# Optimization experiments

Measured on AMD Instinct MI355X. Metric: run time of the kernel, lower is better.

Reference implementation:

```python
import jax, jax.numpy as jnp
import numpy as np

B, Z, H, T = 256, 512, 2048, 16
EPS = 1e-5

def _normalize(v):
    return v / (jnp.linalg.norm(v) + 1e-12)

def setup_inputs() -> dict:
    key = jax.random.key(0)
    ks = jax.random.split(key, 10)
    s = lambda fan: 1.0 / np.sqrt(fan)
    return {
        "z": jax.random.normal(ks[0], (B, Z), dtype=jnp.float32),
        "fc_w": jax.random.normal(ks[1], (Z, Z), dtype=jnp.float32) * s(Z),
        "fc_b": jnp.zeros((Z,), dtype=jnp.float32),
        "fc_u": _normalize(jax.random.normal(ks[2], (Z,), dtype=jnp.float32)),
        "w_ih": jax.random.normal(ks[3], (3 * H, Z), dtype=jnp.float32) * s(Z),
        "w_hh": jax.random.normal(ks[4], (3 * H, H), dtype=jnp.float32) * s(H),
        "b_ih": jnp.zeros((3 * H,), dtype=jnp.float32).at[H:2 * H].set(1.0),  # forget-gate bias init
        "b_hh": jnp.zeros((3 * H,), dtype=jnp.float32),
        "lin_w": jax.random.normal(ks[5], (Z, H), dtype=jnp.float32) * s(H),
        "lin_b": jnp.zeros((Z,), dtype=jnp.float32),
    }

def _spectral_norm(w, u):
    # one torch-style power iteration (u, v treated as constants)
    v = jax.lax.stop_gradient(_normalize(w.T @ u))
    u1 = jax.lax.stop_gradient(_normalize(w @ v))
    sigma = u1 @ (w @ v)
    return w / sigma

def reference(z, fc_w, fc_b, fc_u, w_ih, w_hh, b_ih, b_hh, lin_w, lin_b):
    # spectral-norm linear: h0 = z @ (W/sigma)^T + b
    w_sn = _spectral_norm(fc_w, fc_u)
    x0 = z @ w_sn.T + fc_b                      # [B, Z]
    h0 = jnp.zeros((B, H), dtype=z.dtype)       # initHidden

    def step(carry, _):
        x, h = carry
        gi = x @ w_ih.T + b_ih                  # [B, 3H]
        gh = h @ w_hh.T + b_hh                  # [B, 3H]
        i_r, i_z, i_n = jnp.split(gi, 3, axis=1)
        h_r, h_z, h_n = jnp.split(gh, 3, axis=1)
        r = jax.nn.sigmoid(i_r + h_r)
        u = jax.nn.sigmoid(i_z + h_z)
        n = jnp.tanh(i_n + r * h_n)
        h_new = (1.0 - u) * n + u * h
        x_new = h_new @ lin_w.T + lin_b         # [B, Z] fed back as next input
        return (x_new, h_new), x_new

    _, outs = jax.lax.scan(step, (x0, h0), None, length=T)  # [T, B, Z]

    # per-timestep BatchNorm1d(affine=False), training-mode batch stats
    mean = jnp.mean(outs, axis=1, keepdims=True)
    var = jnp.mean((outs - mean) ** 2, axis=1, keepdims=True)
    y = (outs - mean) / jnp.sqrt(var + EPS)     # [T, B, Z]

    y = jnp.transpose(y, (1, 0, 2))             # [B, T, Z]
    return y.reshape(-1, Z)                     # [B*T, Z]
```

## Files before the change

kernel.cpp:

```cpp
#include <hip/hip_runtime.h>
#include <hip/hip_bf16.h>
#include <cstdint>
#include <cstddef>

#define B_  256
#define Z_  512
#define H_  2048
#define T_  16
#define H3_ 6144

using short8  = __attribute__((ext_vector_type(8))) short;
using bf16x8  = __attribute__((ext_vector_type(8))) __bf16;
using f32x4   = __attribute__((ext_vector_type(4))) float;
using f32x16  = __attribute__((ext_vector_type(16))) float;

__device__ __forceinline__ f32x4 mfma_bf16(short8 a, short8 b, f32x4 c) {
  return __builtin_amdgcn_mfma_f32_16x16x32_bf16(
      __builtin_bit_cast(bf16x8, a), __builtin_bit_cast(bf16x8, b), c, 0, 0, 0);
}
__device__ __forceinline__ f32x16 mfma_bf16_32(short8 a, short8 b, f32x16 c) {
  return __builtin_amdgcn_mfma_f32_32x32x16_bf16(
      __builtin_bit_cast(bf16x8, a), __builtin_bit_cast(bf16x8, b), c, 0, 0, 0);
}

__device__ __forceinline__ unsigned short f2bf(float f) {
  unsigned int u = __builtin_bit_cast(unsigned int, f);
  u = (u + 0x7FFFu + ((u >> 16) & 1u)) >> 16;
  return (unsigned short)u;
}

__device__ __forceinline__ float sigmoidf_(float x) { return 1.0f / (1.0f + __expf(-x)); }

__device__ __forceinline__ int swz(int row, int chunk) {
  return row * 64 + ((chunk ^ (row & 7)) << 3);
}

__global__ __launch_bounds__(256, 1) void gru_step5(
    const unsigned short* __restrict__ A, int K,
    const unsigned short* __restrict__ Wr,
    const unsigned short* __restrict__ Wz,
    const unsigned short* __restrict__ Wn,
    const unsigned short* __restrict__ Whn,
    const float* __restrict__ cr, const float* __restrict__ cz,
    const float* __restrict__ cn, const float* __restrict__ chn,
    float hn_scale,
    const float* __restrict__ h_old,
    float* __restrict__ h_new,
    unsigned short* __restrict__ h_hist)
{
  __shared__ __align__(16) unsigned short sbuf[2][12288];
  __shared__ float LDSf[4][64][33];
  const int bid = blockIdx.x, tid = threadIdx.x;
  const int xcd = bid & 7, rst = bid >> 3;
  const int m_idx = rst & 3, gg = rst >> 2;
  const int grp = gg * 8 + xcd;
  const int m0 = m_idx * 64;
  const int gh0 = grp * 32;
  const int wave = tid >> 6, lane = tid & 63;
  const int kk = wave & 1, gp = wave >> 1;
  const int lh = lane >> 5, l31 = lane & 31;

  const int arow = tid >> 2, ac0 = (tid & 3) * 2;
  const int wrow = tid >> 1, wc0 = (tid & 1) * 4;
  const unsigned short* wsrc =
      (wave == 0) ? Wr : (wave == 1) ? Wz : (wave == 2) ? Wn : Whn;
  const size_t aoff = (size_t)(m0 + arow) * K + ac0 * 8;
  const size_t woff = (size_t)(gh0 + (wrow & 31)) * K + wc0 * 8;
  const int sa_d0 = swz(arow, ac0);
  const int sa_d1 = swz(arow, ac0 + 1);
  const int sw_d0 = 4096 + swz(wrow, wc0 + 0);
  const int sw_d1 = 4096 + swz(wrow, wc0 + 1);
  const int sw_d2 = 4096 + swz(wrow, wc0 + 2);
  const int sw_d3 = 4096 + swz(wrow, wc0 + 3);

  uint4 Aa0, Aa1, Aw0, Aw1, Aw2, Aw3;
  uint4 Ba0, Ba1, Bw0, Bw1, Bw2, Bw3;

#define LDSET(a0, a1, w0, w1, w2, w3, k0)                  \
  {                                                        \
    const int kk_ = (k0);                                  \
    a0 = *(const uint4*)(A    + aoff + kk_);               \
    a1 = *(const uint4*)(A    + aoff + kk_ + 8);           \
    w0 = *(const uint4*)(wsrc + woff + kk_);               \
    w1 = *(const uint4*)(wsrc + woff + kk_ + 8);           \
    w2 = *(const uint4*)(wsrc + woff + kk_ + 16);          \
    w3 = *(const uint4*)(wsrc + woff + kk_ + 24);          \
  }
#define STAGE(s, a0, a1, w0, w1, w2, w3)                   \
  {                                                        \
    unsigned short* b_ = sbuf[s];                          \
    *(uint4*)(b_ + sa_d0) = a0;                            \
    *(uint4*)(b_ + sa_d1) = a1;                            \
    *(uint4*)(b_ + sw_d0) = w0;                            \
    *(uint4*)(b_ + sw_d1) = w1;                            \
    *(uint4*)(b_ + sw_d2) = w2;                            \
    *(uint4*)(b_ + sw_d3) = w3;                            \
  }

  f32x16 acc00 = {}, acc01 = {}, acc10 = {}, acc11 = {};
  const int g0r = (gp * 2) * 32, g1r = (gp * 2 + 1) * 32;

#define COMP(s)                                                            \
  {                                                                        \
    const unsigned short* b_ = sbuf[s];                                    \
    _Pragma("unroll")                                                      \
    for (int ksi = 0; ksi < 2; ++ksi) {                                    \
      const int ch = kk * 4 + ksi * 2 + lh;                                \
      short8 af0 = *(const short8*)(b_ + swz(l31, ch));                    \
      short8 af1 = *(const short8*)(b_ + swz(32 + l31, ch));               \
      short8 wf0 = *(const short8*)(b_ + 4096 + swz(g0r + l31, ch));       \
      short8 wf1 = *(const short8*)(b_ + 4096 + swz(g1r + l31, ch));       \
      acc00 = mfma_bf16_32(af0, wf0, acc00);                               \
      acc01 = mfma_bf16_32(af0, wf1, acc01);                               \
      acc10 = mfma_bf16_32(af1, wf0, acc10);                               \
      acc11 = mfma_bf16_32(af1, wf1, acc11);                               \
    }                                                                      \
  }

  const int nIter = K >> 6;
  LDSET(Aa0, Aa1, Aw0, Aw1, Aw2, Aw3, 0);
  LDSET(Ba0, Ba1, Bw0, Bw1, Bw2, Bw3, 64);
  for (int it = 0; it < nIter; it += 2) {
    STAGE(0, Aa0, Aa1, Aw0, Aw1, Aw2, Aw3);
    __syncthreads();
    { const int kn = (it + 2 < nIter) ? ((it + 2) << 6) : 0;
      LDSET(Aa0, Aa1, Aw0, Aw1, Aw2, Aw3, kn); }
    COMP(0);
    STAGE(1, Ba0, Ba1, Bw0, Bw1, Bw2, Bw3);
    __syncthreads();
    { const int kn = (it + 3 < nIter) ? ((it + 3) << 6) : 64;
      LDSET(Ba0, Ba1, Bw0, Bw1, Bw2, Bw3, kn); }
    COMP(1);
  }
#undef LDSET
#undef STAGE
#undef COMP

  __syncthreads();
  float* red = (float*)sbuf;
#define RSLOT(t, r) ((((gp << 2) | (t)) * 16 + (r)) * 64 + lane)
  if (kk == 1) {
#pragma unroll
    for (int r = 0; r < 16; ++r) red[RSLOT(0, r)] = acc00[r];
#pragma unroll
    for (int r = 0; r < 16; ++r) red[RSLOT(1, r)] = acc01[r];
#pragma unroll
    for (int r = 0; r < 16; ++r) red[RSLOT(2, r)] = acc10[r];
#pragma unroll
    for (int r = 0; r < 16; ++r) red[RSLOT(3, r)] = acc11[r];
  }
  __syncthreads();
  if (kk == 0) {
#pragma unroll
    for (int r = 0; r < 16; ++r) acc00[r] += red[RSLOT(0, r)];
#pragma unroll
    for (int r = 0; r < 16; ++r) acc01[r] += red[RSLOT(1, r)];
#pragma unroll
    for (int r = 0; r < 16; ++r) acc10[r] += red[RSLOT(2, r)];
#pragma unroll
    for (int r = 0; r < 16; ++r) acc11[r] += red[RSLOT(3, r)];
#pragma unroll
    for (int r = 0; r < 16; ++r) {
      const int trow = (r & 3) + 8 * (r >> 2) + 4 * lh;
      LDSf[gp * 2    ][trow     ][l31] = acc00[r];
      LDSf[gp * 2 + 1][trow     ][l31] = acc01[r];
      LDSf[gp * 2    ][32 + trow][l31] = acc10[r];
      LDSf[gp * 2 + 1][32 + trow][l31] = acc11[r];
    }
  }
#undef RSLOT
  __syncthreads();
  {
    const int row = tid >> 2, c0 = (tid & 3) * 8;
    const int grow = m0 + row;
#pragma unroll
    for (int j = 0; j < 8; ++j) {
      const int col = c0 + j;
      const int gcol = gh0 + col;
      const float R   = sigmoidf_(LDSf[0][row][col] + cr[gcol]);
      const float U   = sigmoidf_(LDSf[1][row][col] + cz[gcol]);
      const float HNv = hn_scale * LDSf[3][row][col] + chn[gcol];
      const float Nv  = tanhf(LDSf[2][row][col] + cn[gcol] + R * HNv);
      const float ho  = h_old ? h_old[(size_t)grow * H_ + gcol] : 0.0f;
      const float hv  = (1.0f - U) * Nv + U * ho;
      h_new[(size_t)grow * H_ + gcol]  = hv;
      h_hist[(size_t)grow * H_ + gcol] = f2bf(hv);
    }
  }
}

__global__ __launch_bounds__(256) void gemm_bt(
    const unsigned short* __restrict__ A,
    const unsigned short* __restrict__ Bw,
    int K,
    const float* __restrict__ addsrc, int add_ld,
    const float* __restrict__ bias,
    const float* __restrict__ scale_ptr,
    unsigned short* __restrict__ out_bf,
    float* __restrict__ out_f, int ldo)
{
  __shared__ unsigned short sA[32 * 64];
  __shared__ unsigned short sB[64 * 64];
  const int tid  = threadIdx.x;
  const int m0   = blockIdx.x * 32, n0 = blockIdx.y * 64;
  const int wave = tid >> 6, lane = tid & 63;
  const int wr = wave & 1, wc = wave >> 1;
  const int q = lane >> 4, c16 = lane & 15;
  const int lr = tid >> 3, lc8 = tid & 7;
  f32x4 acc0 = {}, acc1 = {};
  const size_t rowA  = (size_t)(m0 + lr) * K;
  const size_t rowB0 = (size_t)(n0 + lr) * K;
  const size_t rowB1 = (size_t)(n0 + 32 + lr) * K;
  for (int k0 = 0; k0 < K; k0 += 64) {
    const int gc = k0 + lc8 * 8;
    uint4 ra  = *(const uint4*)(A  + rowA  + gc);
    uint4 rb0 = *(const uint4*)(Bw + rowB0 + gc);
    uint4 rb1 = *(const uint4*)(Bw + rowB1 + gc);
    __syncthreads();
    *(uint4*)(sA + swz(lr, lc8))      = ra;
    *(uint4*)(sB + swz(lr, lc8))      = rb0;
    *(uint4*)(sB + swz(32 + lr, lc8)) = rb1;
    __syncthreads();
#pragma unroll
    for (int kk = 0; kk < 2; ++kk) {
      const int arow = wr * 16 + c16;
      short8 af = *(const short8*)(sA + swz(arow, kk * 4 + q));
      const int brow = wc * 32 + c16;
      short8 b0 = *(const short8*)(sB + swz(brow, kk * 4 + q));
      acc0 = mfma_bf16(af, b0, acc0);
      short8 b1 = *(const short8*)(sB + swz(brow + 16, kk * 4 + q));
      acc1 = mfma_bf16(af, b1, acc1);
    }
  }
  const float scale = scale_ptr ? *scale_ptr : 1.0f;
#pragma unroll
  for (int cf = 0; cf < 2; ++cf) {
    f32x4 a = cf ? acc1 : acc0;
#pragma unroll
    for (int v = 0; v < 4; ++v) {
      const int row = m0 + wr * 16 + q * 4 + v;
      const int col = n0 + wc * 32 + cf * 16 + c16;
      float val = a[v] * scale;
      if (addsrc) val += addsrc[(size_t)row * add_ld + col];
      if (bias)   val += bias[col];
      if (out_f)  out_f[(size_t)row * ldo + col] = val;
      if (out_bf) out_bf[(size_t)row * ldo + col] = f2bf(val);
    }
  }
}

__device__ __forceinline__ void dev_gemm64core(
    unsigned short* sA, unsigned short* sB,
    const unsigned short* __restrict__ A,
    const unsigned short* __restrict__ Bw,
    int K,
    const float* __restrict__ addsrc, int add_ld,
    const float* __restrict__ bias,
    unsigned short* __restrict__ out_bf,
    float* __restrict__ out_f, int ldo, int mi, int ni)
{
  const int tid  = threadIdx.x;
  const int m0   = mi * 64, n0 = ni * 64;
  const int wave = tid >> 6, lane = tid & 63;
  const int wr = wave & 1, wc = wave >> 1;
  const int q = lane >> 4, c16 = lane & 15;
  const int lr = tid >> 3, lc8 = tid & 7;
  f32x4 acc[2][2] = {};
  const size_t aoff = (size_t)(m0 + lr) * K;
  const size_t boff = (size_t)(n0 + lr) * K;
  const size_t s32  = (size_t)32 * K;

  uint4 ra0, ra1, rb0, rb1;
  auto LOAD = [&](int k0) {
    const int gc = k0 + lc8 * 8;
    ra0 = *(const uint4*)(A  + aoff + gc);
    ra1 = *(const uint4*)(A  + aoff + s32 + gc);
    rb0 = *(const uint4*)(Bw + boff + gc);
    rb1 = *(const uint4*)(Bw + boff + s32 + gc);
  };

  const int nIter = K >> 6;
  LOAD(0);
  for (int it = 0; it < nIter; ++it) {
    __syncthreads();
    *(uint4*)(sA + swz(lr, lc8))      = ra0;
    *(uint4*)(sA + swz(lr + 32, lc8)) = ra1;
    *(uint4*)(sB + swz(lr, lc8))      = rb0;
    *(uint4*)(sB + swz(lr + 32, lc8)) = rb1;
    __syncthreads();
    if (it + 1 < nIter) LOAD((it + 1) << 6);
#pragma unroll
    for (int kk = 0; kk < 2; ++kk) {
      short8 af0 = *(const short8*)(sA + swz(wr * 32 + c16,      kk * 4 + q));
      short8 af1 = *(const short8*)(sA + swz(wr * 32 + 16 + c16, kk * 4 + q));
      short8 bf0 = *(const short8*)(sB + swz(wc * 32 + c16,      kk * 4 + q));
      short8 bf1 = *(const short8*)(sB + swz(wc * 32 + 16 + c16, kk * 4 + q));
      acc[0][0] = mfma_bf16(af0, bf0, acc[0][0]);
      acc[0][1] = mfma_bf16(af0, bf1, acc[0][1]);
      acc[1][0] = mfma_bf16(af1, bf0, acc[1][0]);
      acc[1][1] = mfma_bf16(af1, bf1, acc[1][1]);
    }
  }
#pragma unroll
  for (int i = 0; i < 2; ++i) {
#pragma unroll
    for (int j = 0; j < 2; ++j) {
#pragma unroll
      for (int v = 0; v < 4; ++v) {
        const int row = m0 + wr * 32 + i * 16 + q * 4 + v;
        const int col = n0 + wc * 32 + j * 16 + c16;
        float val = acc[i][j][v];
        if (addsrc) val += addsrc[(size_t)row * add_ld + col];
        if (bias)   val += bias[col];
        if (out_f)  out_f[(size_t)row * ldo + col] = val;
        if (out_bf) out_bf[(size_t)row * ldo + col] = f2bf(val);
      }
    }
  }
}

__global__ __launch_bounds__(256) void gemm_bt64(
    const unsigned short* __restrict__ A,
    const unsigned short* __restrict__ Bw,
    int K,
    const float* __restrict__ addsrc, int add_ld,
    const float* __restrict__ bias,
    unsigned short* __restrict__ out_bf,
    float* __restrict__ out_f, int ldo)
{
  __shared__ unsigned short sA[64 * 64];
  __shared__ unsigned short sB[64 * 64];
  dev_gemm64core(sA, sB, A, Bw, K, addsrc, add_ld, bias, out_bf, out_f, ldo,
                 blockIdx.x, blockIdx.y);
}

__global__ __launch_bounds__(256) void gemm_wsum(
    const unsigned short* __restrict__ w_ih_q,
    const unsigned short* __restrict__ lin_wT_q,
    const float* __restrict__ w_hh,
    unsigned short* __restrict__ Wsum_r,
    unsigned short* __restrict__ Wsum_z,
    unsigned short* __restrict__ Wn_c)
{
  __shared__ unsigned short sA[64 * 64];
  __shared__ unsigned short sB[64 * 64];
  const int g = blockIdx.y >> 5, ni = blockIdx.y & 31;
  const float* adds = (g < 2) ? (w_hh + (size_t)g * H_ * H_) : nullptr;
  unsigned short* outw = (g == 0) ? Wsum_r : (g == 1) ? Wsum_z : Wn_c;
  dev_gemm64core(sA, sB, w_ih_q + (size_t)g * H_ * Z_, lin_wT_q, Z_,
                 adds, H_, nullptr, outw, nullptr, H_, blockIdx.x, ni);
}

__global__ __launch_bounds__(256) void quant_all(
    const float* __restrict__ z, const float* __restrict__ fc_w,
    const float* __restrict__ w_ih, const float* __restrict__ w_hh,
    const float* __restrict__ lin_w,
    unsigned short* __restrict__ z_q, unsigned short* __restrict__ fc_w_q,
    unsigned short* __restrict__ w_ih_q, unsigned short* __restrict__ w_hhn_q,
    unsigned short* __restrict__ lin_w_q)
{
  const int i = blockIdx.x * 256 + threadIdx.x;
  if (i >= 2195456) return;
  const float4* src; ushort4* dst; int idx;
  if (i < 32768)        { src = (const float4*)z;     dst = (ushort4*)z_q;     idx = i; }
  else if (i < 98304)   { src = (const float4*)fc_w;  dst = (ushort4*)fc_w_q;  idx = i - 32768; }
  else if (i < 884736)  { src = (const float4*)w_ih;  dst = (ushort4*)w_ih_q;  idx = i - 98304; }
  else if (i < 1933312) { src = (const float4*)(w_hh + (size_t)2 * H_ * H_);
                          dst = (ushort4*)w_hhn_q;    idx = i - 884736; }
  else                  { src = (const float4*)lin_w; dst = (ushort4*)lin_w_q; idx = i - 1933312; }
  float4 v = src[idx];
  ushort4 o; o.x = f2bf(v.x); o.y = f2bf(v.y); o.z = f2bf(v.z); o.w = f2bf(v.w);
  dst[idx] = o;
}

__global__ __launch_bounds__(256) void transq(const float* __restrict__ s,
                                              unsigned short* __restrict__ d) {
  __shared__ float tile[32][33];
  const int tx = threadIdx.x & 31, ty = threadIdx.x >> 5;
  const int k0 = blockIdx.x * 32, z0 = blockIdx.y * 32;
#pragma unroll
  for (int j = 0; j < 4; ++j)
    tile[ty + j * 8][tx] = s[(size_t)(z0 + ty + j * 8) * H_ + k0 + tx];
  __syncthreads();
#pragma unroll
  for (int j = 0; j < 4; ++j)
    d[(size_t)(k0 + ty + j * 8) * Z_ + z0 + tx] = f2bf(tile[tx][ty + j * 8]);
}

__global__ void sigma1(const float* __restrict__ W, const float* __restrict__ u,
                       float* __restrict__ t1) {
  __shared__ float part[4][64];
  const int lane = threadIdx.x & 63, wv = threadIdx.x >> 6;
  const int col = blockIdx.x * 64 + lane;
  float s = 0.f;
  for (int r = wv * 128; r < wv * 128 + 128; ++r)
    s += W[(size_t)r * Z_ + col] * u[r];
  part[wv][lane] = s;
  __syncthreads();
  if (wv == 0)
    t1[col] = part[0][lane] + part[1][lane] + part[2][lane] + part[3][lane];
}

__global__ void sigma2(const float* __restrict__ W, const float* __restrict__ t1,
                       float* __restrict__ t2) {
  __shared__ float red[256];
  const int tid = threadIdx.x;
  float p = 0.f;
  for (int c = tid; c < Z_; c += 256) { float v = t1[c]; p += v * v; }
  red[tid] = p;
  __syncthreads();
  for (int s = 128; s > 0; s >>= 1) {
    if (tid < s) red[tid] += red[tid + s];
    __syncthreads();
  }
  const float invn = 1.0f / (sqrtf(red[0]) + 1e-12f);
  const int lane = tid & 63, wv = tid >> 6;
  const int row = blockIdx.x * 4 + wv;
  float s = 0.f;
  for (int c = lane; c < Z_; c += 64) s += W[(size_t)row * Z_ + c] * t1[c];
#pragma unroll
  for (int off = 32; off > 0; off >>= 1) s += __shfl_down(s, off);
  if (lane == 0) t2[row] = s * invn;
}

__global__ void sigma3(const float* __restrict__ t2, float* __restrict__ inv_sig) {
  __shared__ float red[256];
  int t = threadIdx.x;
  float v0 = t2[t], v1 = t2[t + 256];
  red[t] = v0 * v0 + v1 * v1;
  __syncthreads();
  for (int s = 128; s > 0; s >>= 1) {
    if (t < s) red[t] += red[t + s];
    __syncthreads();
  }
  if (t == 0) {
    float s2  = red[0];
    float sig = s2 / (sqrtf(s2) + 1e-12f);
    inv_sig[0] = 1.0f / sig;
  }
}

__global__ __launch_bounds__(256) void dots2_k(
    const float* __restrict__ w, const float* __restrict__ lb,
    const float* __restrict__ b_ih, const float* __restrict__ b_hh,
    float* __restrict__ c0r, float* __restrict__ c0z, float* __restrict__ c0n,
    float* __restrict__ c1r, float* __restrict__ c1z, float* __restrict__ c1n,
    float* __restrict__ chn)
{
  const int wave = threadIdx.x >> 6, lane = threadIdx.x & 63;
#pragma unroll
  for (int i = 0; i < 4; ++i) {
    int row = blockIdx.x * 16 + wave * 4 + i;
    float s = 0.f;
    for (int c = lane; c < Z_; c += 64) s += w[(size_t)row * Z_ + c] * lb[c];
#pragma unroll
    for (int off = 32; off > 0; off >>= 1) s += __shfl_down(s, off);
    if (lane == 0) {
      const int g = row >> 11, j = row & 2047;
      const float bi = b_ih[row], bh = b_hh[row];
      if (g == 0)      { c0r[j] = bi + bh; c1r[j] = bi + bh + s; }
      else if (g == 1) { c0z[j] = bi + bh; c1z[j] = bi + bh + s; }
      else             { c0n[j] = bi;      c1n[j] = bi + s;      chn[j] = bh; }
    }
  }
}

__global__ __launch_bounds__(256) void bn_k(const float* __restrict__ outs,
                                            float* __restrict__ y) {
  __shared__ float s_sum[4][64], s_sq[4][64], s_mean[64], s_inv[64];
  const int t = blockIdx.x, zb = blockIdx.y;
  const int zl = threadIdx.x & 63, bp = threadIdx.x >> 6;
  const int z = zb * 64 + zl;
  float sum = 0.f, sq = 0.f;
  for (int b = bp * 64; b < bp * 64 + 64; ++b) {
    float v = outs[(size_t)(t * 256 + b) * Z_ + z];
    sum += v; sq += v * v;
  }
  s_sum[bp][zl] = sum; s_sq[bp][zl] = sq;
  __syncthreads();
  if (bp == 0) {
    float S = s_sum[0][zl] + s_sum[1][zl] + s_sum[2][zl] + s_sum[3][zl];
    float Q = s_sq[0][zl] + s_sq[1][zl] + s_sq[2][zl] + s_sq[3][zl];
    float mean = S * (1.0f / 256.0f);
    float var  = Q * (1.0f / 256.0f) - mean * mean;
    s_mean[zl] = mean;
    s_inv[zl]  = rsqrtf(var + 1e-5f);
  }
  __syncthreads();
  const float mean = s_mean[zl], inv = s_inv[zl];
  for (int b = bp * 64; b < bp * 64 + 64; ++b) {
    float v = outs[(size_t)(t * 256 + b) * Z_ + z];
    y[(size_t)(b * T_ + t) * Z_ + z] = (v - mean) * inv;
  }
}

extern "C" void kernel_launch(void* const* d_in, const int* in_sizes, int n_in,
                              void* d_out, int out_size, void* d_ws, size_t ws_size,
                              hipStream_t stream) {
  const float* z     = (const float*)d_in[0];
  const float* fc_w  = (const float*)d_in[1];
  const float* fc_b  = (const float*)d_in[2];
  const float* fc_u  = (const float*)d_in[3];
  const float* w_ih  = (const float*)d_in[4];
  const float* w_hh  = (const float*)d_in[5];
  const float* b_ih  = (const float*)d_in[6];
  const float* b_hh  = (const float*)d_in[7];
  const float* lin_w = (const float*)d_in[8];
  const float* lin_b = (const float*)d_in[9];
  float* out = (float*)d_out;

  char* ws = (char*)d_ws;
  size_t off = 0;
  auto alloc = [&](size_t bytes) -> void* {
    off = (off + 255) & ~(size_t)255;
    void* p = ws + off;
    off += bytes;
    return p;
  };
  unsigned short* w_ih_q   = (unsigned short*)alloc((size_t)H3_ * Z_ * 2);
  unsigned short* w_hhn_q  = (unsigned short*)alloc((size_t)H_ * H_ * 2);
  unsigned short* lin_w_q  = (unsigned short*)alloc((size_t)Z_ * H_ * 2);
  unsigned short* lin_wT_q = (unsigned short*)alloc((size_t)Z_ * H_ * 2);
  unsigned short* fc_w_q   = (unsigned short*)alloc((size_t)Z_ * Z_ * 2);
  unsigned short* z_q      = (unsigned short*)alloc((size_t)B_ * Z_ * 2);
  unsigned short* x0_q     = (unsigned short*)alloc((size_t)B_ * Z_ * 2);
  unsigned short* Wsum_r   = (unsigned short*)alloc((size_t)H_ * H_ * 2);
  unsigned short* Wsum_z   = (unsigned short*)alloc((size_t)H_ * H_ * 2);
  unsigned short* Wn_c     = (unsigned short*)alloc((size_t)H_ * H_ * 2);
  unsigned short* Hhist    = (unsigned short*)alloc((size_t)T_ * B_ * H_ * 2);
  float* h_f32 = (float*)alloc((size_t)2 * B_ * H_ * 4);
  float* outs  = (float*)alloc((size_t)T_ * B_ * Z_ * 4);
  float* c0r = (float*)alloc(H_ * 4);
  float* c0z = (float*)alloc(H_ * 4);
  float* c0n = (float*)alloc(H_ * 4);
  float* c1r = (float*)alloc(H_ * 4);
  float* c1z = (float*)alloc(H_ * 4);
  float* c1n = (float*)alloc(H_ * 4);
  float* chn = (float*)alloc(H_ * 4);
  float* t1v = (float*)alloc(Z_ * 4);
  float* t2v = (float*)alloc(Z_ * 4);
  float* invsig = (float*)alloc(256);
  (void)in_sizes; (void)n_in; (void)out_size; (void)ws_size;

  quant_all<<<dim3((2195456 + 255) / 256), 256, 0, stream>>>(
      z, fc_w, w_ih, w_hh, lin_w, z_q, fc_w_q, w_ih_q, w_hhn_q, lin_w_q);
  transq<<<dim3(64, 16), 256, 0, stream>>>(lin_w, lin_wT_q);
  sigma1<<<8, 256, 0, stream>>>(fc_w, fc_u, t1v);
  sigma2<<<128, 256, 0, stream>>>(fc_w, t1v, t2v);
  sigma3<<<1, 256, 0, stream>>>(t2v, invsig);
  dots2_k<<<384, 256, 0, stream>>>(w_ih, lin_b, b_ih, b_hh,
                                   c0r, c0z, c0n, c1r, c1z, c1n, chn);

  gemm_bt<<<dim3(B_ / 32, Z_ / 64), 256, 0, stream>>>(
      z_q, fc_w_q, Z_, nullptr, 0, fc_b, invsig, x0_q, nullptr, Z_);

  gemm_wsum<<<dim3(H_ / 64, 96), 256, 0, stream>>>(
      w_ih_q, lin_wT_q, w_hh, Wsum_r, Wsum_z, Wn_c);

  for (int t = 0; t < T_; ++t) {
    if (t == 0) {
      gru_step5<<<256, 256, 0, stream>>>(
          x0_q, Z_,
          w_ih_q, w_ih_q + (size_t)H_ * Z_, w_ih_q + (size_t)2 * H_ * Z_,
          w_ih_q ,
          c0r, c0z, c0n, chn, 0.0f, nullptr, h_f32, Hhist);
    } else {
      gru_step5<<<256, 256, 0, stream>>>(
          Hhist + (size_t)(t - 1) * B_ * H_, H_,
          Wsum_r, Wsum_z, Wn_c, w_hhn_q,
          c1r, c1z, c1n, chn, 1.0f,
          h_f32 + (size_t)((t - 1) & 1) * B_ * H_,
          h_f32 + (size_t)(t & 1) * B_ * H_,
          Hhist + (size_t)t * B_ * H_);
    }
  }

  gemm_bt64<<<dim3(T_ * B_ / 64, Z_ / 64), 256, 0, stream>>>(
      Hhist, lin_w_q, H_, nullptr, 0, lin_b, nullptr, outs, Z_);

  bn_k<<<dim3(T_, Z_ / 64), 256, 0, stream>>>(outs, out);
}
```

Before: 446.3 us.

## Pre-pack GRU weights into MFMA fragment order and load directly to registers

Weights for the recurrent step are repacked once into the per-lane MFMA operand layout, so each wave loads its B fragments straight from global memory into registers, with no LDS staging. The step kernel goes to 512 threads, one wave per gate and K-half, and only the activation tile goes through shared memory. This removes LDS traffic and barriers for the weight stream. The cost is extra packing work in the preprocessing kernels, an extra packed copy of w_ih, and more register pressure.

```diff
diff --git a/kernel.cpp b/kernel.cpp
--- a/kernel.cpp
+++ b/kernel.cpp
@@ -35,7 +35,13 @@
   return row * 64 + ((chunk ^ (row & 7)) << 3);
 }
 
-__global__ __launch_bounds__(256, 1) void gru_step5(
+__device__ __forceinline__ size_t pidx(int row, int col, int K) {
+  const int grp = row >> 5, prow = row & 31;
+  const int s = col >> 4, lh = (col >> 3) & 1, j = col & 7;
+  return (((size_t)grp * (K >> 4) + s) << 9) + (((lh << 5) | prow) << 3) + j;
+}
+
+__global__ __launch_bounds__(512, 1) void gru_step6(
     const unsigned short* __restrict__ A, int K,
     const unsigned short* __restrict__ Wr,
     const unsigned short* __restrict__ Wz,
@@ -48,7 +54,8 @@
     float* __restrict__ h_new,
     unsigned short* __restrict__ h_hist)
 {
-  __shared__ __align__(16) unsigned short sbuf[2][12288];
+  __shared__ __align__(16) unsigned short sA[2][4096];
+  __shared__ float rawred[8][16][64];
   __shared__ float LDSf[4][64][33];
   const int bid = blockIdx.x, tid = threadIdx.x;
   const int xcd = bid & 7, rst = bid >> 3;
@@ -57,124 +64,76 @@
   const int m0 = m_idx * 64;
   const int gh0 = grp * 32;
   const int wave = tid >> 6, lane = tid & 63;
-  const int kk = wave & 1, gp = wave >> 1;
+  const int gate = wave & 3, kk = wave >> 2;
   const int lh = lane >> 5, l31 = lane & 31;
 
-  const int arow = tid >> 2, ac0 = (tid & 3) * 2;
-  const int wrow = tid >> 1, wc0 = (tid & 1) * 4;
-  const unsigned short* wsrc =
-      (wave == 0) ? Wr : (wave == 1) ? Wz : (wave == 2) ? Wn : Whn;
-  const size_t aoff = (size_t)(m0 + arow) * K + ac0 * 8;
-  const size_t woff = (size_t)(gh0 + (wrow & 31)) * K + wc0 * 8;
-  const int sa_d0 = swz(arow, ac0);
-  const int sa_d1 = swz(arow, ac0 + 1);
-  const int sw_d0 = 4096 + swz(wrow, wc0 + 0);
-  const int sw_d1 = 4096 + swz(wrow, wc0 + 1);
-  const int sw_d2 = 4096 + swz(wrow, wc0 + 2);
-  const int sw_d3 = 4096 + swz(wrow, wc0 + 3);
-
-  uint4 Aa0, Aa1, Aw0, Aw1, Aw2, Aw3;
-  uint4 Ba0, Ba1, Bw0, Bw1, Bw2, Bw3;
-
-#define LDSET(a0, a1, w0, w1, w2, w3, k0)                  \
-  {                                                        \
-    const int kk_ = (k0);                                  \
-    a0 = *(const uint4*)(A    + aoff + kk_);               \
-    a1 = *(const uint4*)(A    + aoff + kk_ + 8);           \
-    w0 = *(const uint4*)(wsrc + woff + kk_);               \
-    w1 = *(const uint4*)(wsrc + woff + kk_ + 8);           \
-    w2 = *(const uint4*)(wsrc + woff + kk_ + 16);          \
-    w3 = *(const uint4*)(wsrc + woff + kk_ + 24);          \
-  }
-#define STAGE(s, a0, a1, w0, w1, w2, w3)                   \
-  {                                                        \
-    unsigned short* b_ = sbuf[s];                          \
-    *(uint4*)(b_ + sa_d0) = a0;                            \
-    *(uint4*)(b_ + sa_d1) = a1;                            \
-    *(uint4*)(b_ + sw_d0) = w0;                            \
-    *(uint4*)(b_ + sw_d1) = w1;                            \
-    *(uint4*)(b_ + sw_d2) = w2;                            \
-    *(uint4*)(b_ + sw_d3) = w3;                            \
-  }
-
-  f32x16 acc00 = {}, acc01 = {}, acc10 = {}, acc11 = {};
-  const int g0r = (gp * 2) * 32, g1r = (gp * 2 + 1) * 32;
-
-#define COMP(s)                                                            \
-  {                                                                        \
-    const unsigned short* b_ = sbuf[s];                                    \
-    _Pragma("unroll")                                                      \
-    for (int ksi = 0; ksi < 2; ++ksi) {                                    \
-      const int ch = kk * 4 + ksi * 2 + lh;                                \
-      short8 af0 = *(const short8*)(b_ + swz(l31, ch));                    \
-      short8 af1 = *(const short8*)(b_ + swz(32 + l31, ch));               \
-      short8 wf0 = *(const short8*)(b_ + 4096 + swz(g0r + l31, ch));       \
-      short8 wf1 = *(const short8*)(b_ + 4096 + swz(g1r + l31, ch));       \
-      acc00 = mfma_bf16_32(af0, wf0, acc00);                               \
-      acc01 = mfma_bf16_32(af0, wf1, acc01);                               \
-      acc10 = mfma_bf16_32(af1, wf0, acc10);                               \
-      acc11 = mfma_bf16_32(af1, wf1, acc11);                               \
-    }                                                                      \
-  }
+  const unsigned short* Wg =
+      (gate == 0) ? Wr : (gate == 1) ? Wz : (gate == 2) ? Wn : Whn;
+  const int ns = K >> 4;
+  const unsigned short* wbase = Wg + (((size_t)grp * ns) << 9) + lane * 8;
+
+  const int arow = tid >> 3, achk = tid & 7;
+  const size_t aoff = (size_t)(m0 + arow) * K + achk * 8;
+  const int sa_d = swz(arow, achk);
+
+  f32x16 acc0 = {}, acc1 = {};
+  uint4 Ar, W0, W1, Wn0, Wn1;
 
   const int nIter = K >> 6;
-  LDSET(Aa0, Aa1, Aw0, Aw1, Aw2, Aw3, 0);
-  LDSET(Ba0, Ba1, Bw0, Bw1, Bw2, Bw3, 64);
-  for (int it = 0; it < nIter; it += 2) {
-    STAGE(0, Aa0, Aa1, Aw0, Aw1, Aw2, Aw3);
-    __syncthreads();
-    { const int kn = (it + 2 < nIter) ? ((it + 2) << 6) : 0;
-      LDSET(Aa0, Aa1, Aw0, Aw1, Aw2, Aw3, kn); }
-    COMP(0);
-    STAGE(1, Ba0, Ba1, Bw0, Bw1, Bw2, Bw3);
-    __syncthreads();
-    { const int kn = (it + 3 < nIter) ? ((it + 3) << 6) : 64;
-      LDSET(Ba0, Ba1, Bw0, Bw1, Bw2, Bw3, kn); }
-    COMP(1);
-  }
-#undef LDSET
-#undef STAGE
-#undef COMP
-
-  __syncthreads();
-  float* red = (float*)sbuf;
-#define RSLOT(t, r) ((((gp << 2) | (t)) * 16 + (r)) * 64 + lane)
+  Ar = *(const uint4*)(A + aoff);
+  {
+    const size_t sb = ((size_t)(kk * 2)) << 9;
+    W0 = *(const uint4*)(wbase + sb);
+    W1 = *(const uint4*)(wbase + sb + 512);
+  }
+  for (int it = 0; it < nIter; ++it) {
+    const int b = it & 1;
+    *(uint4*)(sA[b] + sa_d) = Ar;
+    __syncthreads();
+    if (it + 1 < nIter) {
+      Ar = *(const uint4*)(A + aoff + ((it + 1) << 6));
+      const size_t sb = ((size_t)((it + 1) * 4 + kk * 2)) << 9;
+      Wn0 = *(const uint4*)(wbase + sb);
+      Wn1 = *(const uint4*)(wbase + sb + 512);
+    }
+#pragma unroll
+    for (int ksi = 0; ksi < 2; ++ksi) {
+      const int ch = (kk * 2 + ksi) * 2 + lh;
+      short8 af0 = *(const short8*)(sA[b] + swz(l31, ch));
+      short8 af1 = *(const short8*)(sA[b] + swz(32 + l31, ch));
+      short8 wf = __builtin_bit_cast(short8, ksi ? W1 : W0);
+      acc0 = mfma_bf16_32(af0, wf, acc0);
+      acc1 = mfma_bf16_32(af1, wf, acc1);
+    }
+    W0 = Wn0; W1 = Wn1;
+  }
+
+  __syncthreads();
   if (kk == 1) {
 #pragma unroll
-    for (int r = 0; r < 16; ++r) red[RSLOT(0, r)] = acc00[r];
-#pragma unroll
-    for (int r = 0; r < 16; ++r) red[RSLOT(1, r)] = acc01[r];
-#pragma unroll
-    for (int r = 0; r < 16; ++r) red[RSLOT(2, r)] = acc10[r];
-#pragma unroll
-    for (int r = 0; r < 16; ++r) red[RSLOT(3, r)] = acc11[r];
+    for (int r = 0; r < 16; ++r) rawred[gate * 2    ][r][lane] = acc0[r];
+#pragma unroll
+    for (int r = 0; r < 16; ++r) rawred[gate * 2 + 1][r][lane] = acc1[r];
   }
   __syncthreads();
   if (kk == 0) {
 #pragma unroll
-    for (int r = 0; r < 16; ++r) acc00[r] += red[RSLOT(0, r)];
-#pragma unroll
-    for (int r = 0; r < 16; ++r) acc01[r] += red[RSLOT(1, r)];
-#pragma unroll
-    for (int r = 0; r < 16; ++r) acc10[r] += red[RSLOT(2, r)];
-#pragma unroll
-    for (int r = 0; r < 16; ++r) acc11[r] += red[RSLOT(3, r)];
+    for (int r = 0; r < 16; ++r) acc0[r] += rawred[gate * 2    ][r][lane];
+#pragma unroll
+    for (int r = 0; r < 16; ++r) acc1[r] += rawred[gate * 2 + 1][r][lane];
 #pragma unroll
     for (int r = 0; r < 16; ++r) {
       const int trow = (r & 3) + 8 * (r >> 2) + 4 * lh;
-      LDSf[gp * 2    ][trow     ][l31] = acc00[r];
-      LDSf[gp * 2 + 1][trow     ][l31] = acc01[r];
-      LDSf[gp * 2    ][32 + trow][l31] = acc10[r];
-      LDSf[gp * 2 + 1][32 + trow][l31] = acc11[r];
-    }
-  }
-#undef RSLOT
+      LDSf[gate][trow     ][l31] = acc0[r];
+      LDSf[gate][32 + trow][l31] = acc1[r];
+    }
+  }
   __syncthreads();
   {
-    const int row = tid >> 2, c0 = (tid & 3) * 8;
+    const int row = tid >> 3, c0 = (tid & 7) * 4;
     const int grow = m0 + row;
 #pragma unroll
-    for (int j = 0; j < 8; ++j) {
+    for (int j = 0; j < 4; ++j) {
       const int col = c0 + j;
       const int gcol = gh0 + col;
       const float R   = sigmoidf_(LDSf[0][row][col] + cr[gcol]);
@@ -257,7 +216,7 @@
     const float* __restrict__ addsrc, int add_ld,
     const float* __restrict__ bias,
     unsigned short* __restrict__ out_bf,
-    float* __restrict__ out_f, int ldo, int mi, int ni)
+    float* __restrict__ out_f, int ldo, int mi, int ni, int pack_K)
 {
   const int tid  = threadIdx.x;
   const int m0   = mi * 64, n0 = ni * 64;
@@ -313,7 +272,10 @@
         if (addsrc) val += addsrc[(size_t)row * add_ld + col];
         if (bias)   val += bias[col];
         if (out_f)  out_f[(size_t)row * ldo + col] = val;
-        if (out_bf) out_bf[(size_t)row * ldo + col] = f2bf(val);
+        if (out_bf) {
+          if (pack_K) out_bf[pidx(row, col, pack_K)] = f2bf(val);
+          else        out_bf[(size_t)row * ldo + col] = f2bf(val);
+        }
       }
     }
   }
@@ -331,24 +293,24 @@
   __shared__ unsigned short sA[64 * 64];
   __shared__ unsigned short sB[64 * 64];
   dev_gemm64core(sA, sB, A, Bw, K, addsrc, add_ld, bias, out_bf, out_f, ldo,
-                 blockIdx.x, blockIdx.y);
+                 blockIdx.x, blockIdx.y, 0);
 }
 
 __global__ __launch_bounds__(256) void gemm_wsum(
     const unsigned short* __restrict__ w_ih_q,
     const unsigned short* __restrict__ lin_wT_q,
     const float* __restrict__ w_hh,
-    unsigned short* __restrict__ Wsum_r,
-    unsigned short* __restrict__ Wsum_z,
-    unsigned short* __restrict__ Wn_c)
+    unsigned short* __restrict__ Wsum_r_p,
+    unsigned short* __restrict__ Wsum_z_p,
+    unsigned short* __restrict__ Wsum_n_p)
 {
   __shared__ unsigned short sA[64 * 64];
   __shared__ unsigned short sB[64 * 64];
   const int g = blockIdx.y >> 5, ni = blockIdx.y & 31;
   const float* adds = (g < 2) ? (w_hh + (size_t)g * H_ * H_) : nullptr;
-  unsigned short* outw = (g == 0) ? Wsum_r : (g == 1) ? Wsum_z : Wn_c;
+  unsigned short* outw = (g == 0) ? Wsum_r_p : (g == 1) ? Wsum_z_p : Wsum_n_p;
   dev_gemm64core(sA, sB, w_ih_q + (size_t)g * H_ * Z_, lin_wT_q, Z_,
-                 adds, H_, nullptr, outw, nullptr, H_, blockIdx.x, ni);
+                 adds, H_, nullptr, outw, nullptr, H_, blockIdx.x, ni, H_);
 }
 
 __global__ __launch_bounds__(256) void quant_all(
@@ -356,21 +318,40 @@
     const float* __restrict__ w_ih, const float* __restrict__ w_hh,
     const float* __restrict__ lin_w,
     unsigned short* __restrict__ z_q, unsigned short* __restrict__ fc_w_q,
-    unsigned short* __restrict__ w_ih_q, unsigned short* __restrict__ w_hhn_q,
-    unsigned short* __restrict__ lin_w_q)
+    unsigned short* __restrict__ w_ih_q, unsigned short* __restrict__ w_ih_p,
+    unsigned short* __restrict__ w_hhn_p, unsigned short* __restrict__ lin_w_q)
 {
   const int i = blockIdx.x * 256 + threadIdx.x;
   if (i >= 2195456) return;
-  const float4* src; ushort4* dst; int idx;
-  if (i < 32768)        { src = (const float4*)z;     dst = (ushort4*)z_q;     idx = i; }
-  else if (i < 98304)   { src = (const float4*)fc_w;  dst = (ushort4*)fc_w_q;  idx = i - 32768; }
-  else if (i < 884736)  { src = (const float4*)w_ih;  dst = (ushort4*)w_ih_q;  idx = i - 98304; }
-  else if (i < 1933312) { src = (const float4*)(w_hh + (size_t)2 * H_ * H_);
-                          dst = (ushort4*)w_hhn_q;    idx = i - 884736; }
-  else                  { src = (const float4*)lin_w; dst = (ushort4*)lin_w_q; idx = i - 1933312; }
-  float4 v = src[idx];
-  ushort4 o; o.x = f2bf(v.x); o.y = f2bf(v.y); o.z = f2bf(v.z); o.w = f2bf(v.w);
-  dst[idx] = o;
+  if (i < 32768) {
+    float4 v = ((const float4*)z)[i];
+    ushort4 o; o.x = f2bf(v.x); o.y = f2bf(v.y); o.z = f2bf(v.z); o.w = f2bf(v.w);
+    ((ushort4*)z_q)[i] = o;
+  } else if (i < 98304) {
+    const int idx = i - 32768;
+    float4 v = ((const float4*)fc_w)[idx];
+    ushort4 o; o.x = f2bf(v.x); o.y = f2bf(v.y); o.z = f2bf(v.z); o.w = f2bf(v.w);
+    ((ushort4*)fc_w_q)[idx] = o;
+  } else if (i < 884736) {
+    const int idx = i - 98304;
+    float4 v = ((const float4*)w_ih)[idx];
+    ushort4 o; o.x = f2bf(v.x); o.y = f2bf(v.y); o.z = f2bf(v.z); o.w = f2bf(v.w);
+    ((ushort4*)w_ih_q)[idx] = o;
+    const int row = idx >> 7, k0 = (idx & 127) << 2;
+    const int gate = row >> 11, r2 = row & 2047;
+    *(ushort4*)(w_ih_p + (size_t)gate * 1048576 + pidx(r2, k0, Z_)) = o;
+  } else if (i < 1933312) {
+    const int idx = i - 884736;
+    float4 v = ((const float4*)(w_hh + (size_t)2 * H_ * H_))[idx];
+    ushort4 o; o.x = f2bf(v.x); o.y = f2bf(v.y); o.z = f2bf(v.z); o.w = f2bf(v.w);
+    const int row = idx >> 9, k0 = (idx & 511) << 2;
+    *(ushort4*)(w_hhn_p + pidx(row, k0, H_)) = o;
+  } else {
+    const int idx = i - 1933312;
+    float4 v = ((const float4*)lin_w)[idx];
+    ushort4 o; o.x = f2bf(v.x); o.y = f2bf(v.y); o.z = f2bf(v.z); o.w = f2bf(v.w);
+    ((ushort4*)lin_w_q)[idx] = o;
+  }
 }
 
 __global__ __launch_bounds__(256) void transq(const float* __restrict__ s,
@@ -518,15 +499,16 @@
     return p;
   };
   unsigned short* w_ih_q   = (unsigned short*)alloc((size_t)H3_ * Z_ * 2);
-  unsigned short* w_hhn_q  = (unsigned short*)alloc((size_t)H_ * H_ * 2);
+  unsigned short* w_ih_p   = (unsigned short*)alloc((size_t)H3_ * Z_ * 2);
+  unsigned short* w_hhn_p  = (unsigned short*)alloc((size_t)H_ * H_ * 2);
   unsigned short* lin_w_q  = (unsigned short*)alloc((size_t)Z_ * H_ * 2);
   unsigned short* lin_wT_q = (unsigned short*)alloc((size_t)Z_ * H_ * 2);
   unsigned short* fc_w_q   = (unsigned short*)alloc((size_t)Z_ * Z_ * 2);
   unsigned short* z_q      = (unsigned short*)alloc((size_t)B_ * Z_ * 2);
   unsigned short* x0_q     = (unsigned short*)alloc((size_t)B_ * Z_ * 2);
-  unsigned short* Wsum_r   = (unsigned short*)alloc((size_t)H_ * H_ * 2);
-  unsigned short* Wsum_z   = (unsigned short*)alloc((size_t)H_ * H_ * 2);
-  unsigned short* Wn_c     = (unsigned short*)alloc((size_t)H_ * H_ * 2);
+  unsigned short* Wsum_r_p = (unsigned short*)alloc((size_t)H_ * H_ * 2);
+  unsigned short* Wsum_z_p = (unsigned short*)alloc((size_t)H_ * H_ * 2);
+  unsigned short* Wsum_n_p = (unsigned short*)alloc((size_t)H_ * H_ * 2);
   unsigned short* Hhist    = (unsigned short*)alloc((size_t)T_ * B_ * H_ * 2);
   float* h_f32 = (float*)alloc((size_t)2 * B_ * H_ * 4);
   float* outs  = (float*)alloc((size_t)T_ * B_ * Z_ * 4);
@@ -542,8 +524,8 @@
   float* invsig = (float*)alloc(256);
   (void)in_sizes; (void)n_in; (void)out_size; (void)ws_size;
 
-  quant_all<<<dim3((2195456 + 255) / 256), 256, 0, stream>>>(
-      z, fc_w, w_ih, w_hh, lin_w, z_q, fc_w_q, w_ih_q, w_hhn_q, lin_w_q);
+  quant_all<<<dim3(2195456 / 256), 256, 0, stream>>>(
+      z, fc_w, w_ih, w_hh, lin_w, z_q, fc_w_q, w_ih_q, w_ih_p, w_hhn_p, lin_w_q);
   transq<<<dim3(64, 16), 256, 0, stream>>>(lin_w, lin_wT_q);
   sigma1<<<8, 256, 0, stream>>>(fc_w, fc_u, t1v);
   sigma2<<<128, 256, 0, stream>>>(fc_w, t1v, t2v);
@@ -555,19 +537,19 @@
       z_q, fc_w_q, Z_, nullptr, 0, fc_b, invsig, x0_q, nullptr, Z_);
 
   gemm_wsum<<<dim3(H_ / 64, 96), 256, 0, stream>>>(
-      w_ih_q, lin_wT_q, w_hh, Wsum_r, Wsum_z, Wn_c);
+      w_ih_q, lin_wT_q, w_hh, Wsum_r_p, Wsum_z_p, Wsum_n_p);
 
   for (int t = 0; t < T_; ++t) {
     if (t == 0) {
-      gru_step5<<<256, 256, 0, stream>>>(
+      gru_step6<<<256, 512, 0, stream>>>(
           x0_q, Z_,
-          w_ih_q, w_ih_q + (size_t)H_ * Z_, w_ih_q + (size_t)2 * H_ * Z_,
-          w_ih_q ,
+          w_ih_p, w_ih_p + 1048576, w_ih_p + 2 * 1048576,
+          w_ih_p ,
           c0r, c0z, c0n, chn, 0.0f, nullptr, h_f32, Hhist);
     } else {
-      gru_step5<<<256, 256, 0, stream>>>(
+      gru_step6<<<256, 512, 0, stream>>>(
           Hhist + (size_t)(t - 1) * B_ * H_, H_,
-          Wsum_r, Wsum_z, Wn_c, w_hhn_q,
+          Wsum_r_p, Wsum_z_p, Wsum_n_p, w_hhn_p,
           c1r, c1z, c1n, chn, 1.0f,
           h_f32 + (size_t)((t - 1) & 1) * B_ * H_,
           h_f32 + (size_t)(t & 1) * B_ * H_,
```

Result: slower. 469.0 us (+5.1%).
